# Kernel optimization log

Hardware: AMD Instinct MI355X
Metric: run time of the kernel (lower is better)

## Reference

```python
import jax, jax.numpy as jnp
import numpy as np

N_NODES = 50000
N_EDGES = 800000


def setup_inputs() -> dict:
    key = jax.random.key(0)
    ks = jax.random.split(key, 9)
    d, h, hd = 128, 4, 32
    s = 1.0 / np.sqrt(d)
    return {
        "x": jax.random.normal(ks[0], (N_NODES, d), jnp.float32),
        "edge_index": jax.random.randint(ks[1], (2, N_EDGES), 0, N_NODES, jnp.int32),
        "W0": jax.random.normal(ks[2], (d, d), jnp.float32) * s,
        "att_l0": jax.random.normal(ks[3], (h, hd), jnp.float32) * s,
        "att_r0": jax.random.normal(ks[4], (h, hd), jnp.float32) * s,
        "b0": jnp.zeros((d,), jnp.float32),
        "W1": jax.random.normal(ks[5], (d, d), jnp.float32) * s,
        "att_l1": jax.random.normal(ks[6], (h, hd), jnp.float32) * s,
        "att_r1": jax.random.normal(ks[7], (h, hd), jnp.float32) * s,
        "b1": jnp.zeros((hd,), jnp.float32),
    }


def _gat_layer(x, src, dst, W, att_l, att_r, bias, concat):
    # x: [N, F_in]; W: [H*D, F_in] (torch Linear layout); att_*: [H, D]
    n = x.shape[0]
    h, d = att_l.shape
    hx = (x @ W.T).reshape(n, h, d)                     # [N,H,D]
    al = jnp.einsum('nhd,hd->nh', hx, att_l)            # [N,H]
    ar = jnp.einsum('nhd,hd->nh', hx, att_r)
    att = al[src] + ar[dst]                             # [E,H]
    att = jax.nn.leaky_relu(att, negative_slope=0.2)
    # segment softmax over destination nodes
    m = jax.ops.segment_max(att, dst, num_segments=n)   # [N,H]
    att = jnp.exp(att - m[dst])
    ssum = jax.ops.segment_sum(att, dst, num_segments=n)
    att = att / (ssum[dst] + 1e-9)                      # [E,H]
    msgs = att[:, :, None] * hx[src]                    # [E,H,D]
    out = jax.ops.segment_sum(msgs, dst, num_segments=n)  # [N,H,D]
    if concat:
        out = out.reshape(n, h * d)
    else:
        out = out.mean(axis=1)
    return out + bias


def reference(x, edge_index, W0, att_l0, att_r0, b0, W1, att_l1, att_r1, b1):
    src, dst = edge_index[0], edge_index[1]
    x = _gat_layer(x, src, dst, W0, att_l0, att_r0, b0, concat=True)
    x = jax.nn.relu(x)  # dropout is identity in eval mode
    x = _gat_layer(x, src, dst, W1, att_l1, att_r1, b1, concat=False)
    return x
```

## Files before the change

### kernel.cpp

```cpp
#include <hip/hip_runtime.h>
#include <hip/hip_bf16.h>

#define H 4
#define D 32
#define F 128
#define MAXDEG 64
#define PF 16

typedef __attribute__((ext_vector_type(8))) short bf16x8;
typedef __attribute__((ext_vector_type(4))) float f32x4;

__device__ __forceinline__ short f2bf(float v) {
    __hip_bfloat16 h = __float2bfloat16(v);
    return *reinterpret_cast<short*>(&h);
}
__device__ __forceinline__ float bf2f(short s) {
    __hip_bfloat16 h = *reinterpret_cast<__hip_bfloat16*>(&s);
    return __bfloat162float(h);
}

__device__ __forceinline__
void gemm_body(int bid, int nblocks, const float* __restrict__ X,
               const float* __restrict__ W, const float* __restrict__ attl,
               const float* __restrict__ attr, __hip_bfloat16* __restrict__ HXB,
               float* __restrict__ AL, float* __restrict__ AR, int ntiles) {
    const int wave = threadIdx.x >> 6;
    const int lane = threadIdx.x & 63;
    const int m    = lane & 15;
    const int q    = lane >> 4;
    const int q8   = q * 8;

    bf16x8 Bhi[2][4], Blo[2][4];
#pragma unroll
    for (int j = 0; j < 2; ++j) {
        const int fout = wave * 32 + j * 16 + m;
#pragma unroll
        for (int kc = 0; kc < 4; ++kc) {
            const float* wp = W + (size_t)fout * F + kc * 32 + q8;
            float4 w0 = *reinterpret_cast<const float4*>(wp);
            float4 w1 = *reinterpret_cast<const float4*>(wp + 4);
            float wv[8] = {w0.x, w0.y, w0.z, w0.w, w1.x, w1.y, w1.z, w1.w};
#pragma unroll
            for (int t = 0; t < 8; ++t) {
                short h = f2bf(wv[t]);
                Bhi[j][kc][t] = h;
                Blo[j][kc][t] = f2bf(wv[t] - bf2f(h));
            }
        }
    }
    const float alw0  = attl[wave * 32 + m];
    const float alw16 = attl[wave * 32 + 16 + m];
    const float arw0  = attr[wave * 32 + m];
    const float arw16 = attr[wave * 32 + 16 + m];

    for (int tile = bid; tile < ntiles; tile += nblocks) {
        const int node0 = tile * 16;
        bf16x8 Ahi[4], Alo[4];
        const float* xp = X + (size_t)(node0 + m) * F + q8;
#pragma unroll
        for (int kc = 0; kc < 4; ++kc) {
            float4 x0 = *reinterpret_cast<const float4*>(xp + kc * 32);
            float4 x1 = *reinterpret_cast<const float4*>(xp + kc * 32 + 4);
            float xv[8] = {x0.x, x0.y, x0.z, x0.w, x1.x, x1.y, x1.z, x1.w};
#pragma unroll
            for (int t = 0; t < 8; ++t) {
                short h = f2bf(xv[t]);
                Ahi[kc][t] = h;
                Alo[kc][t] = f2bf(xv[t] - bf2f(h));
            }
        }
        f32x4 acc0 = {0.f, 0.f, 0.f, 0.f};
        f32x4 acc1 = {0.f, 0.f, 0.f, 0.f};
#pragma unroll
        for (int kc = 0; kc < 4; ++kc) {
            acc0 = __builtin_amdgcn_mfma_f32_16x16x32_bf16(Ahi[kc], Bhi[0][kc], acc0, 0, 0, 0);
            acc1 = __builtin_amdgcn_mfma_f32_16x16x32_bf16(Ahi[kc], Bhi[1][kc], acc1, 0, 0, 0);
            acc0 = __builtin_amdgcn_mfma_f32_16x16x32_bf16(Ahi[kc], Blo[0][kc], acc0, 0, 0, 0);
            acc1 = __builtin_amdgcn_mfma_f32_16x16x32_bf16(Ahi[kc], Blo[1][kc], acc1, 0, 0, 0);
            acc0 = __builtin_amdgcn_mfma_f32_16x16x32_bf16(Alo[kc], Bhi[0][kc], acc0, 0, 0, 0);
            acc1 = __builtin_amdgcn_mfma_f32_16x16x32_bf16(Alo[kc], Bhi[1][kc], acc1, 0, 0, 0);
        }
        const int row0 = node0 + q * 4;
        const int col0 = wave * 32 + m;
#pragma unroll
        for (int r = 0; r < 4; ++r) {
            HXB[(size_t)(row0 + r) * F + col0]      = __float2bfloat16(acc0[r]);
            HXB[(size_t)(row0 + r) * F + col0 + 16] = __float2bfloat16(acc1[r]);
            float pal = acc0[r] * alw0 + acc1[r] * alw16;
            float par = acc0[r] * arw0 + acc1[r] * arw16;
#pragma unroll
            for (int o = 1; o < 16; o <<= 1) {
                pal += __shfl_xor(pal, o);
                par += __shfl_xor(par, o);
            }
            if (m == 0) {
                AL[(size_t)(row0 + r) * H + wave] = pal;
                AR[(size_t)(row0 + r) * H + wave] = par;
            }
        }
    }
}

__device__ __forceinline__
void wconv_body(const float* __restrict__ W1, __hip_bfloat16* __restrict__ W1hi,
                __hip_bfloat16* __restrict__ W1lo) {
    for (int i = threadIdx.x; i < F * F; i += 256) {
        float v = W1[i];
        short hi = f2bf(v);
        *reinterpret_cast<short*>(&W1hi[i]) = hi;
        *reinterpret_cast<short*>(&W1lo[i]) = f2bf(v - bf2f(hi));
    }
}

__device__ __forceinline__
void scatter_body(int sbid, const int* __restrict__ ei, int E, int lo, int hi,
                  int* __restrict__ deg, unsigned short* __restrict__ ssrc2u) {
    int base = (sbid * 256 + (int)threadIdx.x) * 4;
    if (base + 3 < E) {
        int4 s4 = *reinterpret_cast<const int4*>(ei + base);
        int4 d4 = *reinterpret_cast<const int4*>(ei + E + base);
        if (d4.x >= lo && d4.x < hi) {
            int s = atomicAdd(&deg[d4.x], 1);
            if (s < MAXDEG) ssrc2u[d4.x * MAXDEG + s] = (unsigned short)s4.x;
        }
        if (d4.y >= lo && d4.y < hi) {
            int s = atomicAdd(&deg[d4.y], 1);
            if (s < MAXDEG) ssrc2u[d4.y * MAXDEG + s] = (unsigned short)s4.y;
        }
        if (d4.z >= lo && d4.z < hi) {
            int s = atomicAdd(&deg[d4.z], 1);
            if (s < MAXDEG) ssrc2u[d4.z * MAXDEG + s] = (unsigned short)s4.z;
        }
        if (d4.w >= lo && d4.w < hi) {
            int s = atomicAdd(&deg[d4.w], 1);
            if (s < MAXDEG) ssrc2u[d4.w * MAXDEG + s] = (unsigned short)s4.w;
        }
    } else {
        for (int e = base; e < E; ++e) {
            int src = ei[e], dst = ei[E + e];
            if (dst >= lo && dst < hi) {
                int s = atomicAdd(&deg[dst], 1);
                if (s < MAXDEG) ssrc2u[dst * MAXDEG + s] = (unsigned short)src;
            }
        }
    }
}

__global__ __launch_bounds__(256)
void k_A(const float* __restrict__ X, const float* __restrict__ W0,
         const float* __restrict__ attl0, const float* __restrict__ attr0,
         __hip_bfloat16* __restrict__ HXB0, float* __restrict__ AL0,
         float* __restrict__ AR0, int ntiles, int gemm_blocks,
         const float* __restrict__ W1, __hip_bfloat16* __restrict__ W1hi,
         __hip_bfloat16* __restrict__ W1lo,
         const int* __restrict__ ei, int E, int nsplit,
         int* __restrict__ deg, unsigned short* __restrict__ ssrc2u) {
    const int bid = blockIdx.x;
    if (bid < gemm_blocks)
        gemm_body(bid, gemm_blocks, X, W0, attl0, attr0, HXB0, AL0, AR0, ntiles);
    else if (bid == gemm_blocks)
        wconv_body(W1, W1hi, W1lo);
    else
        scatter_body(bid - gemm_blocks - 1, ei, E, 0, nsplit, deg, ssrc2u);
}

__device__ __forceinline__
int stage_node(int g, int t, int n, const unsigned short* __restrict__ ssrc2u,
               const int* __restrict__ deg, const float* __restrict__ AL,
               const float4 ar4, int (*sidx)[MAXDEG], float (*sw)[MAXDEG][H]) {
    const int cnt  = min(deg[n], MAXDEG);
    const int rcnt = (cnt + PF - 1) & ~(PF - 1);
    if (t < rcnt) {
        if (t < cnt) {
            int s = ssrc2u[n * MAXDEG + t];
            sidx[g][t] = s;
            float4 al4 = *reinterpret_cast<const float4*>(AL + (size_t)s * H);
            float a0 = al4.x + ar4.x; a0 = a0 > 0.f ? a0 : 0.2f * a0;
            float a1 = al4.y + ar4.y; a1 = a1 > 0.f ? a1 : 0.2f * a1;
            float a2 = al4.z + ar4.z; a2 = a2 > 0.f ? a2 : 0.2f * a2;
            float a3 = al4.w + ar4.w; a3 = a3 > 0.f ? a3 : 0.2f * a3;
            sw[g][t][0] = __expf(a0);
            sw[g][t][1] = __expf(a1);
            sw[g][t][2] = __expf(a2);
            sw[g][t][3] = __expf(a3);
        } else {
            sidx[g][t] = 0;
            sw[g][t][0] = 0.f; sw[g][t][1] = 0.f; sw[g][t][2] = 0.f; sw[g][t][3] = 0.f;
        }
    }
    __builtin_amdgcn_wave_barrier();
    return rcnt;
}

__device__ __forceinline__
void gather_node(int g, int t, int h, int rcnt, const __hip_bfloat16* __restrict__ HXB,
                 const int (*sidx)[MAXDEG], const float (*sw)[MAXDEG][H],
                 float& accx, float& accy, float& wsum) {
    for (int base = 0; base < rcnt; base += PF) {
        __hip_bfloat162 v[PF];
#pragma unroll
        for (int j = 0; j < PF; ++j) {
            int s = sidx[g][base + j];
            v[j] = *reinterpret_cast<const __hip_bfloat162*>(HXB + (size_t)s * F + 2 * t);
        }
#pragma unroll
        for (int j = 0; j < PF; ++j) {
            float w = sw[g][base + j][h];
            float2 f = __bfloat1622float2(v[j]);
            accx += w * f.x;
            accy += w * f.y;
            wsum += w;
        }
    }
}

__device__ __forceinline__
void aggr_gemm_body(int tile, const unsigned short* __restrict__ ssrc2u,
                    const int* __restrict__ deg,
                    const float* __restrict__ AL0, const float* __restrict__ AR0,
                    const __hip_bfloat16* __restrict__ HXB0, const float* __restrict__ b0,
                    const __hip_bfloat16* __restrict__ W1hi, const __hip_bfloat16* __restrict__ W1lo,
                    const float* __restrict__ attl1, const float* __restrict__ attr1,
                    __hip_bfloat16* __restrict__ HXB1, float* __restrict__ AL1,
                    float* __restrict__ AR1) {
    __shared__ float xs[16][132];
    __shared__ int   sidx[4][MAXDEG];
    __shared__ float sw[4][MAXDEG][H];
    const int g = threadIdx.x >> 6;
    const int t = threadIdx.x & 63;
    const int h = t >> 4;
    const int node0 = tile * 16;

    for (int i = 0; i < 4; ++i) {
        const int n = node0 + g * 4 + i;
        const float4 ar4 = *reinterpret_cast<const float4*>(AR0 + (size_t)n * H);
        int rcnt = stage_node(g, t, n, ssrc2u, deg, AL0, ar4, sidx, sw);
        float accx = 0.f, accy = 0.f, wsum = 0.f;
        gather_node(g, t, h, rcnt, HXB0, sidx, sw, accx, accy, wsum);
        float inv = 1.f / (wsum + 1e-9f);
        const int row = g * 4 + i;
        xs[row][2 * t]     = fmaxf(accx * inv + b0[2 * t], 0.f);
        xs[row][2 * t + 1] = fmaxf(accy * inv + b0[2 * t + 1], 0.f);
        __builtin_amdgcn_wave_barrier();
    }
    __syncthreads();

    const int wave = g;
    const int m  = t & 15;
    const int q  = t >> 4;
    const int q8 = q * 8;

    bf16x8 Bhi[2][4], Blo[2][4];
#pragma unroll
    for (int j = 0; j < 2; ++j) {
        const int fout = wave * 32 + j * 16 + m;
#pragma unroll
        for (int kc = 0; kc < 4; ++kc) {
            Bhi[j][kc] = *reinterpret_cast<const bf16x8*>(W1hi + (size_t)fout * F + kc * 32 + q8);
            Blo[j][kc] = *reinterpret_cast<const bf16x8*>(W1lo + (size_t)fout * F + kc * 32 + q8);
        }
    }
    bf16x8 Ahi[4], Alo[4];
#pragma unroll
    for (int kc = 0; kc < 4; ++kc) {
        const float* xp = &xs[m][kc * 32 + q8];
        float4 x0 = *reinterpret_cast<const float4*>(xp);
        float4 x1 = *reinterpret_cast<const float4*>(xp + 4);
        float xv[8] = {x0.x, x0.y, x0.z, x0.w, x1.x, x1.y, x1.z, x1.w};
#pragma unroll
        for (int u = 0; u < 8; ++u) {
            short hi = f2bf(xv[u]);
            Ahi[kc][u] = hi;
            Alo[kc][u] = f2bf(xv[u] - bf2f(hi));
        }
    }
    f32x4 acc0 = {0.f, 0.f, 0.f, 0.f};
    f32x4 acc1 = {0.f, 0.f, 0.f, 0.f};
#pragma unroll
    for (int kc = 0; kc < 4; ++kc) {
        acc0 = __builtin_amdgcn_mfma_f32_16x16x32_bf16(Ahi[kc], Bhi[0][kc], acc0, 0, 0, 0);
        acc1 = __builtin_amdgcn_mfma_f32_16x16x32_bf16(Ahi[kc], Bhi[1][kc], acc1, 0, 0, 0);
        acc0 = __builtin_amdgcn_mfma_f32_16x16x32_bf16(Ahi[kc], Blo[0][kc], acc0, 0, 0, 0);
        acc1 = __builtin_amdgcn_mfma_f32_16x16x32_bf16(Ahi[kc], Blo[1][kc], acc1, 0, 0, 0);
        acc0 = __builtin_amdgcn_mfma_f32_16x16x32_bf16(Alo[kc], Bhi[0][kc], acc0, 0, 0, 0);
        acc1 = __builtin_amdgcn_mfma_f32_16x16x32_bf16(Alo[kc], Bhi[1][kc], acc1, 0, 0, 0);
    }
    const float alw0  = attl1[wave * 32 + m];
    const float alw16 = attl1[wave * 32 + 16 + m];
    const float arw0  = attr1[wave * 32 + m];
    const float arw16 = attr1[wave * 32 + 16 + m];
    const int row0 = node0 + q * 4;
    const int col0 = wave * 32 + m;
#pragma unroll
    for (int r = 0; r < 4; ++r) {
        HXB1[(size_t)(row0 + r) * F + col0]      = __float2bfloat16(acc0[r]);
        HXB1[(size_t)(row0 + r) * F + col0 + 16] = __float2bfloat16(acc1[r]);
        float pal = acc0[r] * alw0 + acc1[r] * alw16;
        float par = acc0[r] * arw0 + acc1[r] * arw16;
#pragma unroll
        for (int o = 1; o < 16; o <<= 1) {
            pal += __shfl_xor(pal, o);
            par += __shfl_xor(par, o);
        }
        if (m == 0) {
            AL1[(size_t)(row0 + r) * H + wave] = pal;
            AR1[(size_t)(row0 + r) * H + wave] = par;
        }
    }
}

__global__ __launch_bounds__(256)
void k_B(const int* __restrict__ ei, int E, int nsplit, int scatter_blocks,
         int* __restrict__ deg, unsigned short* __restrict__ ssrc2u,
         const float* __restrict__ AL0, const float* __restrict__ AR0,
         const __hip_bfloat16* __restrict__ HXB0, const float* __restrict__ b0,
         const __hip_bfloat16* __restrict__ W1hi, const __hip_bfloat16* __restrict__ W1lo,
         const float* __restrict__ attl1, const float* __restrict__ attr1,
         __hip_bfloat16* __restrict__ HXB1, float* __restrict__ AL1,
         float* __restrict__ AR1, int N) {
    const int bid = blockIdx.x;
    if (bid < scatter_blocks)
        scatter_body(bid, ei, E, nsplit, N, deg, ssrc2u);
    else
        aggr_gemm_body(bid - scatter_blocks, ssrc2u, deg, AL0, AR0, HXB0, b0,
                       W1hi, W1lo, attl1, attr1, HXB1, AL1, AR1);
}

__global__ __launch_bounds__(256)
void k_C(int tile0, const unsigned short* __restrict__ ssrc2u, const int* __restrict__ deg,
         const float* __restrict__ AL0, const float* __restrict__ AR0,
         const __hip_bfloat16* __restrict__ HXB0, const float* __restrict__ b0,
         const __hip_bfloat16* __restrict__ W1hi, const __hip_bfloat16* __restrict__ W1lo,
         const float* __restrict__ attl1, const float* __restrict__ attr1,
         __hip_bfloat16* __restrict__ HXB1, float* __restrict__ AL1,
         float* __restrict__ AR1) {
    aggr_gemm_body(tile0 + blockIdx.x, ssrc2u, deg, AL0, AR0, HXB0, b0,
                   W1hi, W1lo, attl1, attr1, HXB1, AL1, AR1);
}

__global__ __launch_bounds__(256)
void k_D(const unsigned short* __restrict__ ssrc2u, const int* __restrict__ deg,
         const float* __restrict__ AL, const float* __restrict__ AR,
         const __hip_bfloat16* __restrict__ HXB, const float* __restrict__ bias,
         float* __restrict__ out, int N) {
    __shared__ int   sidx[4][MAXDEG];
    __shared__ float sw[4][MAXDEG][H];
    const int g = threadIdx.x >> 6;
    const int t = threadIdx.x & 63;
    const int n = blockIdx.x * 4 + g;
    if (n >= N) return;
    const int h = t >> 4;
    const float4 ar4 = *reinterpret_cast<const float4*>(AR + (size_t)n * H);
    int rcnt = stage_node(g, t, n, ssrc2u, deg, AL, ar4, sidx, sw);
    float accx = 0.f, accy = 0.f, wsum = 0.f;
    gather_node(g, t, h, rcnt, HXB, sidx, sw, accx, accy, wsum);
    float inv = 1.f / (wsum + 1e-9f);
    float vx = accx * inv, vy = accy * inv;
    vx += __shfl_xor(vx, 16); vx += __shfl_xor(vx, 32);
    vy += __shfl_xor(vy, 16); vy += __shfl_xor(vy, 32);
    if (t < 16) {
        float2 o;
        o.x = 0.25f * vx + bias[2 * t];
        o.y = 0.25f * vy + bias[2 * t + 1];
        *reinterpret_cast<float2*>(out + (size_t)n * D + 2 * t) = o;
    }
}

extern "C" void kernel_launch(void* const* d_in, const int* in_sizes, int n_in,
                              void* d_out, int out_size, void* d_ws, size_t ws_size,
                              hipStream_t stream) {
    const float* x     = (const float*)d_in[0];
    const int*   ei    = (const int*)d_in[1];
    const float* W0    = (const float*)d_in[2];
    const float* attl0 = (const float*)d_in[3];
    const float* attr0 = (const float*)d_in[4];
    const float* b0    = (const float*)d_in[5];
    const float* W1    = (const float*)d_in[6];
    const float* attl1 = (const float*)d_in[7];
    const float* attr1 = (const float*)d_in[8];
    const float* b1    = (const float*)d_in[9];

    const int N = in_sizes[0] / F;
    const int E = in_sizes[1] / 2;
    const int ntiles = N / 16;
    const int tsplit = ntiles / 2;
    const int nsplit = tsplit * 16;

    char* p = (char*)d_ws;
    __hip_bfloat16* HXB0 = (__hip_bfloat16*)p;  p += (size_t)N * F * 2;
    __hip_bfloat16* HXB1 = (__hip_bfloat16*)p;  p += (size_t)N * F * 2;
    __hip_bfloat16* W1hi = (__hip_bfloat16*)p;  p += (size_t)F * F * 2;
    __hip_bfloat16* W1lo = (__hip_bfloat16*)p;  p += (size_t)F * F * 2;
    float* AL0 = (float*)p;                     p += (size_t)N * H * 4;
    float* AR0 = (float*)p;                     p += (size_t)N * H * 4;
    float* AL1 = (float*)p;                     p += (size_t)N * H * 4;
    float* AR1 = (float*)p;                     p += (size_t)N * H * 4;
    unsigned short* ssrc2u = (unsigned short*)p; p += (size_t)N * MAXDEG * 2;
    int* deg = (int*)p;

    hipMemsetAsync(deg, 0, (size_t)N * sizeof(int), stream);

    const int gemm_blocks    = 625;
    const int scatter_blocks = (E / 4 + 255) / 256;

    k_A<<<gemm_blocks + 1 + scatter_blocks, 256, 0, stream>>>(
        x, W0, attl0, attr0, HXB0, AL0, AR0, ntiles, gemm_blocks,
        W1, W1hi, W1lo, ei, E, nsplit, deg, ssrc2u);

    k_B<<<scatter_blocks + tsplit, 256, 0, stream>>>(
        ei, E, nsplit, scatter_blocks, deg, ssrc2u,
        AL0, AR0, HXB0, b0, W1hi, W1lo, attl1, attr1, HXB1, AL1, AR1, N);

    k_C<<<ntiles - tsplit, 256, 0, stream>>>(
        tsplit, ssrc2u, deg, AL0, AR0, HXB0, b0, W1hi, W1lo,
        attl1, attr1, HXB1, AL1, AR1);

    k_D<<<(N + 3) / 4, 256, 0, stream>>>(ssrc2u, deg, AL1, AR1, HXB1, b1,
                                         (float*)d_out, N);
}
```

Before: 237.2 us.

## Split scatter into three node ranges and interleave with GEMM and aggregation kernels

The adjacency scatter pass is split into three destination-node ranges instead of two. Each range is built in the same launch that runs the GEMM or aggregation work for the preceding range, so graph construction overlaps with compute. Blocks alternate odd/even between scatter and compute roles so both kinds of work are co-resident on the device. The cost is one extra launch and an extra full read of the edge list for the added scatter pass, with some idle blocks where the two roles have unequal counts.

Result: slower. 283.0 us (+19.3%).

```diff
diff --git a/kernel.cpp b/kernel.cpp
--- a/kernel.cpp
+++ b/kernel.cpp
@@ -144,24 +144,6 @@
             }
         }
     }
-}
-
-__global__ __launch_bounds__(256)
-void k_A(const float* __restrict__ X, const float* __restrict__ W0,
-         const float* __restrict__ attl0, const float* __restrict__ attr0,
-         __hip_bfloat16* __restrict__ HXB0, float* __restrict__ AL0,
-         float* __restrict__ AR0, int ntiles, int gemm_blocks,
-         const float* __restrict__ W1, __hip_bfloat16* __restrict__ W1hi,
-         __hip_bfloat16* __restrict__ W1lo,
-         const int* __restrict__ ei, int E, int nsplit,
-         int* __restrict__ deg, unsigned short* __restrict__ ssrc2u) {
-    const int bid = blockIdx.x;
-    if (bid < gemm_blocks)
-        gemm_body(bid, gemm_blocks, X, W0, attl0, attr0, HXB0, AL0, AR0, ntiles);
-    else if (bid == gemm_blocks)
-        wconv_body(W1, W1hi, W1lo);
-    else
-        scatter_body(bid - gemm_blocks - 1, ei, E, 0, nsplit, deg, ssrc2u);
 }
 
 __device__ __forceinline__
@@ -310,39 +292,66 @@
 }
 
 __global__ __launch_bounds__(256)
-void k_B(const int* __restrict__ ei, int E, int nsplit, int scatter_blocks,
+void k1(const float* __restrict__ X, const float* __restrict__ W0,
+        const float* __restrict__ attl0, const float* __restrict__ attr0,
+        __hip_bfloat16* __restrict__ HXB0, float* __restrict__ AL0,
+        float* __restrict__ AR0, int ntiles, int gemm_blocks,
+        const float* __restrict__ W1, __hip_bfloat16* __restrict__ W1hi,
+        __hip_bfloat16* __restrict__ W1lo,
+        const int* __restrict__ ei, int E, int scatter_blocks, int hi0,
+        int* __restrict__ deg, unsigned short* __restrict__ ssrc2u) {
+    const int bid = blockIdx.x;
+    if (bid & 1) {
+        const int s = bid >> 1;
+        if (s < scatter_blocks) scatter_body(s, ei, E, 0, hi0, deg, ssrc2u);
+    } else {
+        const int g = bid >> 1;
+        if (g < gemm_blocks)
+            gemm_body(g, gemm_blocks, X, W0, attl0, attr0, HXB0, AL0, AR0, ntiles);
+        else if (g == gemm_blocks)
+            wconv_body(W1, W1hi, W1lo);
+    }
+}
+
+__global__ __launch_bounds__(256)
+void k23(int tile0, int ntchunk, const int* __restrict__ ei, int E,
+         int scatter_blocks, int lo, int hi,
          int* __restrict__ deg, unsigned short* __restrict__ ssrc2u,
          const float* __restrict__ AL0, const float* __restrict__ AR0,
          const __hip_bfloat16* __restrict__ HXB0, const float* __restrict__ b0,
          const __hip_bfloat16* __restrict__ W1hi, const __hip_bfloat16* __restrict__ W1lo,
          const float* __restrict__ attl1, const float* __restrict__ attr1,
          __hip_bfloat16* __restrict__ HXB1, float* __restrict__ AL1,
-         float* __restrict__ AR1, int N) {
+         float* __restrict__ AR1) {
     const int bid = blockIdx.x;
-    if (bid < scatter_blocks)
-        scatter_body(bid, ei, E, nsplit, N, deg, ssrc2u);
-    else
-        aggr_gemm_body(bid - scatter_blocks, ssrc2u, deg, AL0, AR0, HXB0, b0,
-                       W1hi, W1lo, attl1, attr1, HXB1, AL1, AR1);
+    if (bid & 1) {
+        const int s = bid >> 1;
+        if (s < scatter_blocks) scatter_body(s, ei, E, lo, hi, deg, ssrc2u);
+    } else {
+        const int t = bid >> 1;
+        if (t < ntchunk)
+            aggr_gemm_body(tile0 + t, ssrc2u, deg, AL0, AR0, HXB0, b0,
+                           W1hi, W1lo, attl1, attr1, HXB1, AL1, AR1);
+    }
 }
 
 __global__ __launch_bounds__(256)
-void k_C(int tile0, const unsigned short* __restrict__ ssrc2u, const int* __restrict__ deg,
-         const float* __restrict__ AL0, const float* __restrict__ AR0,
-         const __hip_bfloat16* __restrict__ HXB0, const float* __restrict__ b0,
-         const __hip_bfloat16* __restrict__ W1hi, const __hip_bfloat16* __restrict__ W1lo,
-         const float* __restrict__ attl1, const float* __restrict__ attr1,
-         __hip_bfloat16* __restrict__ HXB1, float* __restrict__ AL1,
-         float* __restrict__ AR1) {
+void k4(int tile0, const unsigned short* __restrict__ ssrc2u, const int* __restrict__ deg,
+        const float* __restrict__ AL0, const float* __restrict__ AR0,
+        const __hip_bfloat16* __restrict__ HXB0, const float* __restrict__ b0,
+        const __hip_bfloat16* __restrict__ W1hi, const __hip_bfloat16* __restrict__ W1lo,
+        const float* __restrict__ attl1, const float* __restrict__ attr1,
+        __hip_bfloat16* __restrict__ HXB1, float* __restrict__ AL1,
+        float* __restrict__ AR1) {
     aggr_gemm_body(tile0 + blockIdx.x, ssrc2u, deg, AL0, AR0, HXB0, b0,
                    W1hi, W1lo, attl1, attr1, HXB1, AL1, AR1);
 }
 
 __global__ __launch_bounds__(256)
-void k_D(const unsigned short* __restrict__ ssrc2u, const int* __restrict__ deg,
-         const float* __restrict__ AL, const float* __restrict__ AR,
-         const __hip_bfloat16* __restrict__ HXB, const float* __restrict__ bias,
-         float* __restrict__ out, int N) {
+void k5(const unsigned short* __restrict__ ssrc2u, const int* __restrict__ deg,
+        const float* __restrict__ AL, const float* __restrict__ AR,
+        const __hip_bfloat16* __restrict__ HXB, const float* __restrict__ bias,
+        float* __restrict__ out, int N) {
     __shared__ int   sidx[4][MAXDEG];
     __shared__ float sw[4][MAXDEG][H];
     const int g = threadIdx.x >> 6;
@@ -383,8 +392,11 @@
     const int N = in_sizes[0] / F;
     const int E = in_sizes[1] / 2;
     const int ntiles = N / 16;
-    const int tsplit = ntiles / 2;
-    const int nsplit = tsplit * 16;
+
+    const int tA = ntiles / 3;
+    const int tB = 2 * ntiles / 3;
+    const int n1 = tA * 16;
+    const int n2 = tB * 16;
 
     char* p = (char*)d_ws;
     __hip_bfloat16* HXB0 = (__hip_bfloat16*)p;  p += (size_t)N * F * 2;
@@ -403,18 +415,33 @@
     const int gemm_blocks    = 625;
     const int scatter_blocks = (E / 4 + 255) / 256;
 
-    k_A<<<gemm_blocks + 1 + scatter_blocks, 256, 0, stream>>>(
-        x, W0, attl0, attr0, HXB0, AL0, AR0, ntiles, gemm_blocks,
-        W1, W1hi, W1lo, ei, E, nsplit, deg, ssrc2u);
-
-    k_B<<<scatter_blocks + tsplit, 256, 0, stream>>>(
-        ei, E, nsplit, scatter_blocks, deg, ssrc2u,
-        AL0, AR0, HXB0, b0, W1hi, W1lo, attl1, attr1, HXB1, AL1, AR1, N);
-
-    k_C<<<ntiles - tsplit, 256, 0, stream>>>(
-        tsplit, ssrc2u, deg, AL0, AR0, HXB0, b0, W1hi, W1lo,
-        attl1, attr1, HXB1, AL1, AR1);
-
-    k_D<<<(N + 3) / 4, 256, 0, stream>>>(ssrc2u, deg, AL1, AR1, HXB1, b1,
-                                         (float*)d_out, N);
-}
+    {
+        int grid = 2 * ((gemm_blocks + 1) > scatter_blocks ? (gemm_blocks + 1)
+                                                           : scatter_blocks);
+        k1<<<grid, 256, 0, stream>>>(x, W0, attl0, attr0, HXB0, AL0, AR0,
+                                     ntiles, gemm_blocks, W1, W1hi, W1lo,
+                                     ei, E, scatter_blocks, n1, deg, ssrc2u);
+    }
+
+    {
+        int ntchunk = tA;
+        int grid = 2 * (ntchunk > scatter_blocks ? ntchunk : scatter_blocks);
+        k23<<<grid, 256, 0, stream>>>(0, ntchunk, ei, E, scatter_blocks, n1, n2,
+                                      deg, ssrc2u, AL0, AR0, HXB0, b0,
+                                      W1hi, W1lo, attl1, attr1, HXB1, AL1, AR1);
+    }
+
+    {
+        int ntchunk = tB - tA;
+        int grid = 2 * (ntchunk > scatter_blocks ? ntchunk : scatter_blocks);
+        k23<<<grid, 256, 0, stream>>>(tA, ntchunk, ei, E, scatter_blocks, n2, N,
+                                      deg, ssrc2u, AL0, AR0, HXB0, b0,
+                                      W1hi, W1lo, attl1, attr1, HXB1, AL1, AR1);
+    }
+
+    k4<<<ntiles - tB, 256, 0, stream>>>(tB, ssrc2u, deg, AL0, AR0, HXB0, b0,
+                                        W1hi, W1lo, attl1, attr1, HXB1, AL1, AR1);
+
+    k5<<<(N + 3) / 4, 256, 0, stream>>>(ssrc2u, deg, AL1, AR1, HXB1, b1,
+                                        (float*)d_out, N);
+}
```

## Unfuse layer-1 aggregation from GEMM and scatter full edge list upfront

Applied to the files above, without the earlier changes.

The whole CSR scatter now runs in the first kernel, with scatter and GEMM blocks interleaved by block parity, so the split scatter across two kernels is gone. The fused aggregate+GEMM tile kernel is split into a separate aggregation kernel that writes fp32 activations to a workspace buffer and a standalone persistent MFMA GEMM kernel that reads them back. Workspace buffers for the two layers are shared. This trades an extra round trip of the 50000x128 fp32 hidden activations through global memory for simpler, higher-occupancy kernels and better overlap of scatter atomics with the GEMM.

New measurement: 226.2 us. 1.05x faster.

```diff
diff --git a/kernel.cpp b/kernel.cpp
--- a/kernel.cpp
+++ b/kernel.cpp
@@ -113,55 +113,49 @@
 }
 
 __device__ __forceinline__
-void scatter_body(int sbid, const int* __restrict__ ei, int E, int lo, int hi,
+void scatter_body(int sbid, const int* __restrict__ ei, int E,
                   int* __restrict__ deg, unsigned short* __restrict__ ssrc2u) {
     int base = (sbid * 256 + (int)threadIdx.x) * 4;
     if (base + 3 < E) {
         int4 s4 = *reinterpret_cast<const int4*>(ei + base);
         int4 d4 = *reinterpret_cast<const int4*>(ei + E + base);
-        if (d4.x >= lo && d4.x < hi) {
-            int s = atomicAdd(&deg[d4.x], 1);
-            if (s < MAXDEG) ssrc2u[d4.x * MAXDEG + s] = (unsigned short)s4.x;
-        }
-        if (d4.y >= lo && d4.y < hi) {
-            int s = atomicAdd(&deg[d4.y], 1);
-            if (s < MAXDEG) ssrc2u[d4.y * MAXDEG + s] = (unsigned short)s4.y;
-        }
-        if (d4.z >= lo && d4.z < hi) {
-            int s = atomicAdd(&deg[d4.z], 1);
-            if (s < MAXDEG) ssrc2u[d4.z * MAXDEG + s] = (unsigned short)s4.z;
-        }
-        if (d4.w >= lo && d4.w < hi) {
-            int s = atomicAdd(&deg[d4.w], 1);
-            if (s < MAXDEG) ssrc2u[d4.w * MAXDEG + s] = (unsigned short)s4.w;
-        }
+        int s0 = atomicAdd(&deg[d4.x], 1);
+        int s1 = atomicAdd(&deg[d4.y], 1);
+        int s2 = atomicAdd(&deg[d4.z], 1);
+        int s3 = atomicAdd(&deg[d4.w], 1);
+        if (s0 < MAXDEG) ssrc2u[d4.x * MAXDEG + s0] = (unsigned short)s4.x;
+        if (s1 < MAXDEG) ssrc2u[d4.y * MAXDEG + s1] = (unsigned short)s4.y;
+        if (s2 < MAXDEG) ssrc2u[d4.z * MAXDEG + s2] = (unsigned short)s4.z;
+        if (s3 < MAXDEG) ssrc2u[d4.w * MAXDEG + s3] = (unsigned short)s4.w;
     } else {
         for (int e = base; e < E; ++e) {
             int src = ei[e], dst = ei[E + e];
-            if (dst >= lo && dst < hi) {
-                int s = atomicAdd(&deg[dst], 1);
-                if (s < MAXDEG) ssrc2u[dst * MAXDEG + s] = (unsigned short)src;
-            }
+            int s = atomicAdd(&deg[dst], 1);
+            if (s < MAXDEG) ssrc2u[dst * MAXDEG + s] = (unsigned short)src;
         }
     }
 }
 
 __global__ __launch_bounds__(256)
-void k_A(const float* __restrict__ X, const float* __restrict__ W0,
-         const float* __restrict__ attl0, const float* __restrict__ attr0,
-         __hip_bfloat16* __restrict__ HXB0, float* __restrict__ AL0,
-         float* __restrict__ AR0, int ntiles, int gemm_blocks,
-         const float* __restrict__ W1, __hip_bfloat16* __restrict__ W1hi,
-         __hip_bfloat16* __restrict__ W1lo,
-         const int* __restrict__ ei, int E, int nsplit,
-         int* __restrict__ deg, unsigned short* __restrict__ ssrc2u) {
+void k_pre(const float* __restrict__ X, const float* __restrict__ W0,
+           const float* __restrict__ attl0, const float* __restrict__ attr0,
+           __hip_bfloat16* __restrict__ HXB, float* __restrict__ AL,
+           float* __restrict__ AR, int ntiles, int gemm_blocks,
+           const float* __restrict__ W1, __hip_bfloat16* __restrict__ W1hi,
+           __hip_bfloat16* __restrict__ W1lo,
+           const int* __restrict__ ei, int E, int scatter_blocks,
+           int* __restrict__ deg, unsigned short* __restrict__ ssrc2u) {
     const int bid = blockIdx.x;
-    if (bid < gemm_blocks)
-        gemm_body(bid, gemm_blocks, X, W0, attl0, attr0, HXB0, AL0, AR0, ntiles);
-    else if (bid == gemm_blocks)
-        wconv_body(W1, W1hi, W1lo);
-    else
-        scatter_body(bid - gemm_blocks - 1, ei, E, 0, nsplit, deg, ssrc2u);
+    if (bid & 1) {
+        const int s = bid >> 1;
+        if (s < scatter_blocks) scatter_body(s, ei, E, deg, ssrc2u);
+    } else {
+        const int g = bid >> 1;
+        if (g < gemm_blocks)
+            gemm_body(g, gemm_blocks, X, W0, attl0, attr0, HXB, AL, AR, ntiles);
+        else if (g == gemm_blocks)
+            wconv_body(W1, W1hi, W1lo);
+    }
 }
 
 __device__ __forceinline__
@@ -214,41 +208,40 @@
     }
 }
 
-__device__ __forceinline__
-void aggr_gemm_body(int tile, const unsigned short* __restrict__ ssrc2u,
-                    const int* __restrict__ deg,
-                    const float* __restrict__ AL0, const float* __restrict__ AR0,
-                    const __hip_bfloat16* __restrict__ HXB0, const float* __restrict__ b0,
-                    const __hip_bfloat16* __restrict__ W1hi, const __hip_bfloat16* __restrict__ W1lo,
-                    const float* __restrict__ attl1, const float* __restrict__ attr1,
-                    __hip_bfloat16* __restrict__ HXB1, float* __restrict__ AL1,
-                    float* __restrict__ AR1) {
-    __shared__ float xs[16][132];
+__global__ __launch_bounds__(256)
+void k_aggr0(const unsigned short* __restrict__ ssrc2u, const int* __restrict__ deg,
+             const float* __restrict__ AL, const float* __restrict__ AR,
+             const __hip_bfloat16* __restrict__ HXB, const float* __restrict__ bias,
+             float* __restrict__ out, int N) {
     __shared__ int   sidx[4][MAXDEG];
     __shared__ float sw[4][MAXDEG][H];
     const int g = threadIdx.x >> 6;
     const int t = threadIdx.x & 63;
+    const int n = blockIdx.x * 4 + g;
+    if (n >= N) return;
     const int h = t >> 4;
-    const int node0 = tile * 16;
-
-    for (int i = 0; i < 4; ++i) {
-        const int n = node0 + g * 4 + i;
-        const float4 ar4 = *reinterpret_cast<const float4*>(AR0 + (size_t)n * H);
-        int rcnt = stage_node(g, t, n, ssrc2u, deg, AL0, ar4, sidx, sw);
-        float accx = 0.f, accy = 0.f, wsum = 0.f;
-        gather_node(g, t, h, rcnt, HXB0, sidx, sw, accx, accy, wsum);
-        float inv = 1.f / (wsum + 1e-9f);
-        const int row = g * 4 + i;
-        xs[row][2 * t]     = fmaxf(accx * inv + b0[2 * t], 0.f);
-        xs[row][2 * t + 1] = fmaxf(accy * inv + b0[2 * t + 1], 0.f);
-        __builtin_amdgcn_wave_barrier();
-    }
-    __syncthreads();
-
-    const int wave = g;
-    const int m  = t & 15;
-    const int q  = t >> 4;
-    const int q8 = q * 8;
+    const float4 ar4 = *reinterpret_cast<const float4*>(AR + (size_t)n * H);
+    int rcnt = stage_node(g, t, n, ssrc2u, deg, AL, ar4, sidx, sw);
+    float accx = 0.f, accy = 0.f, wsum = 0.f;
+    gather_node(g, t, h, rcnt, HXB, sidx, sw, accx, accy, wsum);
+    float inv = 1.f / (wsum + 1e-9f);
+    float2 o;
+    o.x = fmaxf(accx * inv + bias[2 * t], 0.f);
+    o.y = fmaxf(accy * inv + bias[2 * t + 1], 0.f);
+    *reinterpret_cast<float2*>(out + (size_t)n * F + 2 * t) = o;
+}
+
+__global__ __launch_bounds__(256)
+void k_gemm1(const float* __restrict__ X, const __hip_bfloat16* __restrict__ W1hi,
+             const __hip_bfloat16* __restrict__ W1lo,
+             const float* __restrict__ attl, const float* __restrict__ attr,
+             __hip_bfloat16* __restrict__ HXB, float* __restrict__ AL,
+             float* __restrict__ AR, int ntiles) {
+    const int wave = threadIdx.x >> 6;
+    const int lane = threadIdx.x & 63;
+    const int m    = lane & 15;
+    const int q    = lane >> 4;
+    const int q8   = q * 8;
 
     bf16x8 Bhi[2][4], Blo[2][4];
 #pragma unroll
@@ -260,89 +253,64 @@
             Blo[j][kc] = *reinterpret_cast<const bf16x8*>(W1lo + (size_t)fout * F + kc * 32 + q8);
         }
     }
-    bf16x8 Ahi[4], Alo[4];
-#pragma unroll
-    for (int kc = 0; kc < 4; ++kc) {
-        const float* xp = &xs[m][kc * 32 + q8];
-        float4 x0 = *reinterpret_cast<const float4*>(xp);
-        float4 x1 = *reinterpret_cast<const float4*>(xp + 4);
-        float xv[8] = {x0.x, x0.y, x0.z, x0.w, x1.x, x1.y, x1.z, x1.w};
-#pragma unroll
-        for (int u = 0; u < 8; ++u) {
-            short hi = f2bf(xv[u]);
-            Ahi[kc][u] = hi;
-            Alo[kc][u] = f2bf(xv[u] - bf2f(hi));
-        }
-    }
-    f32x4 acc0 = {0.f, 0.f, 0.f, 0.f};
-    f32x4 acc1 = {0.f, 0.f, 0.f, 0.f};
-#pragma unroll
-    for (int kc = 0; kc < 4; ++kc) {
-        acc0 = __builtin_amdgcn_mfma_f32_16x16x32_bf16(Ahi[kc], Bhi[0][kc], acc0, 0, 0, 0);
-        acc1 = __builtin_amdgcn_mfma_f32_16x16x32_bf16(Ahi[kc], Bhi[1][kc], acc1, 0, 0, 0);
-        acc0 = __builtin_amdgcn_mfma_f32_16x16x32_bf16(Ahi[kc], Blo[0][kc], acc0, 0, 0, 0);
-        acc1 = __builtin_amdgcn_mfma_f32_16x16x32_bf16(Ahi[kc], Blo[1][kc], acc1, 0, 0, 0);
-        acc0 = __builtin_amdgcn_mfma_f32_16x16x32_bf16(Alo[kc], Bhi[0][kc], acc0, 0, 0, 0);
-        acc1 = __builtin_amdgcn_mfma_f32_16x16x32_bf16(Alo[kc], Bhi[1][kc], acc1, 0, 0, 0);
-    }
-    const float alw0  = attl1[wave * 32 + m];
-    const float alw16 = attl1[wave * 32 + 16 + m];
-    const float arw0  = attr1[wave * 32 + m];
-    const float arw16 = attr1[wave * 32 + 16 + m];
-    const int row0 = node0 + q * 4;
-    const int col0 = wave * 32 + m;
-#pragma unroll
-    for (int r = 0; r < 4; ++r) {
-        HXB1[(size_t)(row0 + r) * F + col0]      = __float2bfloat16(acc0[r]);
-        HXB1[(size_t)(row0 + r) * F + col0 + 16] = __float2bfloat16(acc1[r]);
-        float pal = acc0[r] * alw0 + acc1[r] * alw16;
-        float par = acc0[r] * arw0 + acc1[r] * arw16;
-#pragma unroll
-        for (int o = 1; o < 16; o <<= 1) {
-            pal += __shfl_xor(pal, o);
-            par += __shfl_xor(par, o);
-        }
-        if (m == 0) {
-            AL1[(size_t)(row0 + r) * H + wave] = pal;
-            AR1[(size_t)(row0 + r) * H + wave] = par;
+    const float alw0  = attl[wave * 32 + m];
+    const float alw16 = attl[wave * 32 + 16 + m];
+    const float arw0  = attr[wave * 32 + m];
+    const float arw16 = attr[wave * 32 + 16 + m];
+
+    for (int tile = blockIdx.x; tile < ntiles; tile += gridDim.x) {
+        const int node0 = tile * 16;
+        bf16x8 Ahi[4], Alo[4];
+        const float* xp = X + (size_t)(node0 + m) * F + q8;
+#pragma unroll
+        for (int kc = 0; kc < 4; ++kc) {
+            float4 x0 = *reinterpret_cast<const float4*>(xp + kc * 32);
+            float4 x1 = *reinterpret_cast<const float4*>(xp + kc * 32 + 4);
+            float xv[8] = {x0.x, x0.y, x0.z, x0.w, x1.x, x1.y, x1.z, x1.w};
+#pragma unroll
+            for (int t = 0; t < 8; ++t) {
+                short h = f2bf(xv[t]);
+                Ahi[kc][t] = h;
+                Alo[kc][t] = f2bf(xv[t] - bf2f(h));
+            }
+        }
+        f32x4 acc0 = {0.f, 0.f, 0.f, 0.f};
+        f32x4 acc1 = {0.f, 0.f, 0.f, 0.f};
+#pragma unroll
+        for (int kc = 0; kc < 4; ++kc) {
+            acc0 = __builtin_amdgcn_mfma_f32_16x16x32_bf16(Ahi[kc], Bhi[0][kc], acc0, 0, 0, 0);
+            acc1 = __builtin_amdgcn_mfma_f32_16x16x32_bf16(Ahi[kc], Bhi[1][kc], acc1, 0, 0, 0);
+            acc0 = __builtin_amdgcn_mfma_f32_16x16x32_bf16(Ahi[kc], Blo[0][kc], acc0, 0, 0, 0);
+            acc1 = __builtin_amdgcn_mfma_f32_16x16x32_bf16(Ahi[kc], Blo[1][kc], acc1, 0, 0, 0);
+            acc0 = __builtin_amdgcn_mfma_f32_16x16x32_bf16(Alo[kc], Bhi[0][kc], acc0, 0, 0, 0);
+            acc1 = __builtin_amdgcn_mfma_f32_16x16x32_bf16(Alo[kc], Bhi[1][kc], acc1, 0, 0, 0);
+        }
+        const int row0 = node0 + q * 4;
+        const int col0 = wave * 32 + m;
+#pragma unroll
+        for (int r = 0; r < 4; ++r) {
+            HXB[(size_t)(row0 + r) * F + col0]      = __float2bfloat16(acc0[r]);
+            HXB[(size_t)(row0 + r) * F + col0 + 16] = __float2bfloat16(acc1[r]);
+            float pal = acc0[r] * alw0 + acc1[r] * alw16;
+            float par = acc0[r] * arw0 + acc1[r] * arw16;
+#pragma unroll
+            for (int o = 1; o < 16; o <<= 1) {
+                pal += __shfl_xor(pal, o);
+                par += __shfl_xor(par, o);
+            }
+            if (m == 0) {
+                AL[(size_t)(row0 + r) * H + wave] = pal;
+                AR[(size_t)(row0 + r) * H + wave] = par;
+            }
         }
     }
 }
 
 __global__ __launch_bounds__(256)
-void k_B(const int* __restrict__ ei, int E, int nsplit, int scatter_blocks,
-         int* __restrict__ deg, unsigned short* __restrict__ ssrc2u,
-         const float* __restrict__ AL0, const float* __restrict__ AR0,
-         const __hip_bfloat16* __restrict__ HXB0, const float* __restrict__ b0,
-         const __hip_bfloat16* __restrict__ W1hi, const __hip_bfloat16* __restrict__ W1lo,
-         const float* __restrict__ attl1, const float* __restrict__ attr1,
-         __hip_bfloat16* __restrict__ HXB1, float* __restrict__ AL1,
-         float* __restrict__ AR1, int N) {
-    const int bid = blockIdx.x;
-    if (bid < scatter_blocks)
-        scatter_body(bid, ei, E, nsplit, N, deg, ssrc2u);
-    else
-        aggr_gemm_body(bid - scatter_blocks, ssrc2u, deg, AL0, AR0, HXB0, b0,
-                       W1hi, W1lo, attl1, attr1, HXB1, AL1, AR1);
-}
-
-__global__ __launch_bounds__(256)
-void k_C(int tile0, const unsigned short* __restrict__ ssrc2u, const int* __restrict__ deg,
-         const float* __restrict__ AL0, const float* __restrict__ AR0,
-         const __hip_bfloat16* __restrict__ HXB0, const float* __restrict__ b0,
-         const __hip_bfloat16* __restrict__ W1hi, const __hip_bfloat16* __restrict__ W1lo,
-         const float* __restrict__ attl1, const float* __restrict__ attr1,
-         __hip_bfloat16* __restrict__ HXB1, float* __restrict__ AL1,
-         float* __restrict__ AR1) {
-    aggr_gemm_body(tile0 + blockIdx.x, ssrc2u, deg, AL0, AR0, HXB0, b0,
-                   W1hi, W1lo, attl1, attr1, HXB1, AL1, AR1);
-}
-
-__global__ __launch_bounds__(256)
-void k_D(const unsigned short* __restrict__ ssrc2u, const int* __restrict__ deg,
-         const float* __restrict__ AL, const float* __restrict__ AR,
-         const __hip_bfloat16* __restrict__ HXB, const float* __restrict__ bias,
-         float* __restrict__ out, int N) {
+void k_aggr1(const unsigned short* __restrict__ ssrc2u, const int* __restrict__ deg,
+             const float* __restrict__ AL, const float* __restrict__ AR,
+             const __hip_bfloat16* __restrict__ HXB, const float* __restrict__ bias,
+             float* __restrict__ out, int N) {
     __shared__ int   sidx[4][MAXDEG];
     __shared__ float sw[4][MAXDEG][H];
     const int g = threadIdx.x >> 6;
@@ -383,18 +351,14 @@
     const int N = in_sizes[0] / F;
     const int E = in_sizes[1] / 2;
     const int ntiles = N / 16;
-    const int tsplit = ntiles / 2;
-    const int nsplit = tsplit * 16;
 
     char* p = (char*)d_ws;
-    __hip_bfloat16* HXB0 = (__hip_bfloat16*)p;  p += (size_t)N * F * 2;
-    __hip_bfloat16* HXB1 = (__hip_bfloat16*)p;  p += (size_t)N * F * 2;
+    __hip_bfloat16* HXB  = (__hip_bfloat16*)p;  p += (size_t)N * F * 2;
+    float* X1  = (float*)p;                     p += (size_t)N * F * 4;
     __hip_bfloat16* W1hi = (__hip_bfloat16*)p;  p += (size_t)F * F * 2;
     __hip_bfloat16* W1lo = (__hip_bfloat16*)p;  p += (size_t)F * F * 2;
-    float* AL0 = (float*)p;                     p += (size_t)N * H * 4;
-    float* AR0 = (float*)p;                     p += (size_t)N * H * 4;
-    float* AL1 = (float*)p;                     p += (size_t)N * H * 4;
-    float* AR1 = (float*)p;                     p += (size_t)N * H * 4;
+    float* AL  = (float*)p;                     p += (size_t)N * H * 4;
+    float* AR  = (float*)p;                     p += (size_t)N * H * 4;
     unsigned short* ssrc2u = (unsigned short*)p; p += (size_t)N * MAXDEG * 2;
     int* deg = (int*)p;
 
@@ -402,19 +366,18 @@
 
     const int gemm_blocks    = 625;
     const int scatter_blocks = (E / 4 + 255) / 256;
-
-    k_A<<<gemm_blocks + 1 + scatter_blocks, 256, 0, stream>>>(
-        x, W0, attl0, attr0, HXB0, AL0, AR0, ntiles, gemm_blocks,
-        W1, W1hi, W1lo, ei, E, nsplit, deg, ssrc2u);
-
-    k_B<<<scatter_blocks + tsplit, 256, 0, stream>>>(
-        ei, E, nsplit, scatter_blocks, deg, ssrc2u,
-        AL0, AR0, HXB0, b0, W1hi, W1lo, attl1, attr1, HXB1, AL1, AR1, N);
-
-    k_C<<<ntiles - tsplit, 256, 0, stream>>>(
-        tsplit, ssrc2u, deg, AL0, AR0, HXB0, b0, W1hi, W1lo,
-        attl1, attr1, HXB1, AL1, AR1);
-
-    k_D<<<(N + 3) / 4, 256, 0, stream>>>(ssrc2u, deg, AL1, AR1, HXB1, b1,
-                                         (float*)d_out, N);
-}
+    const int grid_pre = 2 * (scatter_blocks > gemm_blocks + 1 ? scatter_blocks
+                                                               : gemm_blocks + 1);
+
+    k_pre<<<grid_pre, 256, 0, stream>>>(x, W0, attl0, attr0, HXB, AL, AR,
+                                        ntiles, gemm_blocks, W1, W1hi, W1lo,
+                                        ei, E, scatter_blocks, deg, ssrc2u);
+
+    k_aggr0<<<(N + 3) / 4, 256, 0, stream>>>(ssrc2u, deg, AL, AR, HXB, b0, X1, N);
+
+    k_gemm1<<<gemm_blocks, 256, 0, stream>>>(X1, W1hi, W1lo, attl1, attr1,
+                                             HXB, AL, AR, ntiles);
+
+    k_aggr1<<<(N + 3) / 4, 256, 0, stream>>>(ssrc2u, deg, AL, AR, HXB, b1,
+                                             (float*)d_out, N);
+}
```
